# Kernel optimization log

Measured on AMD Instinct MI355X. Metric: run time of the kernel, lower is better.

Reference implementation:

```python
import jax, jax.numpy as jnp
import numpy as np

MARGIN = 1.0  # from init_kwargs
B, H, W, P = 64, 512, 640, 100000


def setup_inputs() -> dict:
    key = jax.random.key(0)
    k0, k1, k2, k3, k4, k5 = jax.random.split(key, 6)
    return {
        "inp": jax.random.normal(k0, (B, 1, H, W), dtype=jnp.float32),
        "x_A": jax.random.randint(k1, (B, P), 0, W, dtype=jnp.int32),
        "y_A": jax.random.randint(k2, (B, P), 0, H, dtype=jnp.int32),
        "x_B": jax.random.randint(k3, (B, P), 0, W, dtype=jnp.int32),
        "y_B": jax.random.randint(k4, (B, P), 0, H, dtype=jnp.int32),
        "ordinal": jax.random.randint(k5, (B, P), 0, 3, dtype=jnp.int32),
    }


def reference(inp, x_A, y_A, x_B, y_B, ordinal):
    # inp: [B,1,H,W]; point coords: [B,P]; ordinal in {0,1,2} -> gt in {-1,0,1}
    depth = inp[:, 0]                                   # [B,H,W]
    bidx = jnp.arange(depth.shape[0])[:, None]          # [B,1]
    z_A = depth[bidx, y_A, x_A]                         # [B,P] gather
    z_B = depth[bidx, y_B, x_B]                         # [B,P] gather
    gt = (ordinal - 1).astype(depth.dtype)              # {-1,0,1}
    mask = jnp.abs(gt)
    zd = z_A - z_B
    m = jnp.asarray(MARGIN, depth.dtype)
    # ordered pairs: log(1+exp(-min(gt*zd, m))); equal pairs: max(zd^2, m^2)
    loss = mask * jnp.log(1.0 + jnp.exp(-jnp.minimum(gt * zd, m))) \
         + (1.0 - mask) * jnp.maximum(zd * zd, m * m)
    n_point_total = depth.shape[0] * x_A.shape[1]
    return jnp.sum(loss) / n_point_total
```

## Files before the change

kernel.cpp:

```cpp
#include <hip/hip_runtime.h>


constexpr int B = 64;
constexpr int H = 512;
constexpr int W = 640;
constexpr int P = 100000;
constexpr int SEGS = 8;
constexpr int SEGP = P / SEGS;
constexpr int NT = 512;
constexpr int G4 = SEGP / 4;
constexpr int KG = (G4 + NT - 1) / NT;
constexpr int TAIL_T = G4 - (KG - 1) * NT;
constexpr int KS = KG * 4;
constexpr int SROWS = 48;
constexpr int NS = (H + SROWS - 1) / SROWS;
constexpr int SELEMS = SROWS * W;
constexpr int LELEMS = (H - (NS - 1) * SROWS) * W;
constexpr int PF = SELEMS / (NT * 4);
constexpr int PF_LAST = LELEMS / (NT * 4);
constexpr int NBLK = B * SEGS;
constexpr float INV_N = 1.0f / (float)(B * P);

typedef float vfloat4 __attribute__((ext_vector_type(4)));
typedef int vint4 __attribute__((ext_vector_type(4)));

__device__ __forceinline__ unsigned bf16_rnd(float f) {
    return (__builtin_bit_cast(unsigned, f) + 0x8000u) >> 16;
}

__global__ __attribute__((amdgpu_flat_work_group_size(NT, NT),
                          amdgpu_waves_per_eu(2, 2)))
void rdc_kernel(
        const float* __restrict__ depth,
        const vint4* __restrict__ xA4, const vint4* __restrict__ yA4,
        const vint4* __restrict__ xB4, const vint4* __restrict__ yB4,
        const vint4* __restrict__ ord4,
        float* __restrict__ partials) {
    __shared__ unsigned short stripe[SELEMS];
    __shared__ float wsum[8];

    int j = blockIdx.x;
    int x = j & 7;
    int g = j >> 3;
    int b = ((g >> 3) << 3) | x;
    int c = g & 7;
    int t = threadIdx.x;

    const float* slab = depth + (size_t)b * (H * W);
    int base_i4 = (b * P + c * SEGP) >> 2;

    int offA[KS], offB[KS];
    unsigned zAB[KS];
    unsigned rankW = 0u;
    unsigned signW = 0u;
    #pragma unroll
    for (int k = 0; k < KG; ++k) {
        int gl = k * NT + t;
        if (k == KG - 1 && gl >= G4) gl = G4 - 1;
        int gi = base_i4 + gl;
        vint4 xa = __builtin_nontemporal_load(&xA4[gi]);
        vint4 ya = __builtin_nontemporal_load(&yA4[gi]);
        vint4 xb = __builtin_nontemporal_load(&xB4[gi]);
        vint4 yb = __builtin_nontemporal_load(&yB4[gi]);
        vint4 od = __builtin_nontemporal_load(&ord4[gi]);
        int s0 = 4 * k;
        offA[s0+0] = ya.x * W + xa.x;  offB[s0+0] = yb.x * W + xb.x;
        offA[s0+1] = ya.y * W + xa.y;  offB[s0+1] = yb.y * W + xb.y;
        offA[s0+2] = ya.z * W + xa.z;  offB[s0+2] = yb.z * W + xb.z;
        offA[s0+3] = ya.w * W + xa.w;  offB[s0+3] = yb.w * W + xb.w;
        rankW |= (unsigned)(od.x != 1) << (s0+0);
        rankW |= (unsigned)(od.y != 1) << (s0+1);
        rankW |= (unsigned)(od.z != 1) << (s0+2);
        rankW |= (unsigned)(od.w != 1) << (s0+3);
        signW |= (unsigned)(od.x == 2) << (s0+0);
        signW |= (unsigned)(od.y == 2) << (s0+1);
        signW |= (unsigned)(od.z == 2) << (s0+2);
        signW |= (unsigned)(od.w == 2) << (s0+3);
        zAB[s0+0] = 0u; zAB[s0+1] = 0u; zAB[s0+2] = 0u; zAB[s0+3] = 0u;
    }

    vfloat4 pf[PF];
    #pragma unroll
    for (int i = 0; i < PF; ++i)
        pf[i] = *(const vfloat4*)(slab + ((i * NT + t) << 2));
    #pragma unroll
    for (int i = 0; i < PF; ++i) {
        uint2 pk;
        pk.x = bf16_rnd(pf[i].x) | (bf16_rnd(pf[i].y) << 16);
        pk.y = bf16_rnd(pf[i].z) | (bf16_rnd(pf[i].w) << 16);
        *(uint2*)&stripe[(i * NT + t) << 2] = pk;
    }
    __syncthreads();

    for (int s = 0; s < NS; ++s) {
        int npf = (s + 1 < NS) ? ((s + 1 == NS - 1) ? PF_LAST : PF) : 0;
        int gbase = (s + 1) * SELEMS;
        #pragma unroll
        for (int i = 0; i < PF; ++i)
            if (i < npf)
                pf[i] = *(const vfloat4*)(slab + gbase + ((i * NT + t) << 2));

        unsigned base = (unsigned)(s * SELEMS);
        unsigned span = (s == NS - 1) ? (unsigned)LELEMS : (unsigned)SELEMS;
        #pragma unroll
        for (int k = 0; k < KS; ++k) {
            unsigned la = (unsigned)offA[k] - base;
            unsigned va = (unsigned)stripe[la < span ? la : 0u];
            zAB[k] = (la < span) ? ((zAB[k] & 0xFFFF0000u) | va) : zAB[k];
            unsigned lb = (unsigned)offB[k] - base;
            unsigned vb = (unsigned)stripe[lb < span ? lb : 0u];
            zAB[k] = (lb < span) ? ((zAB[k] & 0x0000FFFFu) | (vb << 16)) : zAB[k];
        }
        __syncthreads();

        if (npf) {
            #pragma unroll
            for (int i = 0; i < PF; ++i)
                if (i < npf) {
                    uint2 pk;
                    pk.x = bf16_rnd(pf[i].x) | (bf16_rnd(pf[i].y) << 16);
                    pk.y = bf16_rnd(pf[i].z) | (bf16_rnd(pf[i].w) << 16);
                    *(uint2*)&stripe[(i * NT + t) << 2] = pk;
                }
            __syncthreads();
        }
    }

    float acc = 0.0f;
    #pragma unroll
    for (int k = 0; k < KG; ++k) {
        float gmask = (k < KG - 1 || t < TAIL_T) ? 1.0f : 0.0f;
        #pragma unroll
        for (int m = 0; m < 4; ++m) {
            int s = 4 * k + m;
            float za = __builtin_bit_cast(float, zAB[s] << 16);
            float zb = __builtin_bit_cast(float, zAB[s] & 0xFFFF0000u);
            float zd = za - zb;
            unsigned rb = (rankW >> s) & 1u;
            unsigned sb = (signW >> s) & 1u;
            float gzd = sb ? zd : -zd;
            float lr = __logf(1.0f + __expf(-fminf(gzd, 1.0f)));
            float le = fmaxf(zd * zd, 1.0f);
            acc += gmask * (rb ? lr : le);
        }
    }

    #pragma unroll
    for (int o = 32; o > 0; o >>= 1)
        acc += __shfl_down(acc, o, 64);
    int lane = t & 63;
    int wid  = t >> 6;
    if (lane == 0) wsum[wid] = acc;
    __syncthreads();
    if (wid == 0 && lane == 0) {
        float v = 0.0f;
        #pragma unroll
        for (int w = 0; w < 8; ++w) v += wsum[w];
        partials[j] = v;
    }
}

__global__ __launch_bounds__(256) void rdc_finalize(
        const float* __restrict__ partials, float* __restrict__ out, int n) {
    float acc = 0.0f;
    for (int k = threadIdx.x; k < n; k += 256)
        acc += partials[k];
    #pragma unroll
    for (int o = 32; o > 0; o >>= 1)
        acc += __shfl_down(acc, o, 64);
    __shared__ float wsum[4];
    int lane = threadIdx.x & 63;
    int wid  = threadIdx.x >> 6;
    if (lane == 0) wsum[wid] = acc;
    __syncthreads();
    if (wid == 0 && lane == 0)
        out[0] = (wsum[0] + wsum[1] + wsum[2] + wsum[3]) * INV_N;
}

extern "C" void kernel_launch(void* const* d_in, const int* in_sizes, int n_in,
                              void* d_out, int out_size, void* d_ws, size_t ws_size,
                              hipStream_t stream) {
    const float* depth = (const float*)d_in[0];
    const vint4* xA4 = (const vint4*)d_in[1];
    const vint4* yA4 = (const vint4*)d_in[2];
    const vint4* xB4 = (const vint4*)d_in[3];
    const vint4* yB4 = (const vint4*)d_in[4];
    const vint4* ord4 = (const vint4*)d_in[5];
    float* out = (float*)d_out;

    float* partials = (float*)d_ws;
    rdc_kernel<<<NBLK, NT, 0, stream>>>(depth, xA4, yA4, xB4, yB4, ord4, partials);
    rdc_finalize<<<1, 256, 0, stream>>>(partials, out, NBLK);
}
```

Measured before the change: 293.5 us.

## Double-buffer bf16 depth stripes and shrink stripe height with more segments

```diff
diff --git a/kernel.cpp b/kernel.cpp
--- a/kernel.cpp
+++ b/kernel.cpp
@@ -5,19 +5,19 @@
 constexpr int H = 512;
 constexpr int W = 640;
 constexpr int P = 100000;
-constexpr int SEGS = 8;
+constexpr int SEGS = 10;
 constexpr int SEGP = P / SEGS;
 constexpr int NT = 512;
 constexpr int G4 = SEGP / 4;
 constexpr int KG = (G4 + NT - 1) / NT;
 constexpr int TAIL_T = G4 - (KG - 1) * NT;
 constexpr int KS = KG * 4;
-constexpr int SROWS = 48;
+constexpr int SROWS = 24;
 constexpr int NS = (H + SROWS - 1) / SROWS;
 constexpr int SELEMS = SROWS * W;
 constexpr int LELEMS = (H - (NS - 1) * SROWS) * W;
-constexpr int PF = SELEMS / (NT * 4);
-constexpr int PF_LAST = LELEMS / (NT * 4);
+constexpr int F4_FULL = SELEMS / 4;
+constexpr int F4_LAST = LELEMS / 4;
 constexpr int NBLK = B * SEGS;
 constexpr float INV_N = 1.0f / (float)(B * P);
 
@@ -28,25 +28,24 @@
     return (__builtin_bit_cast(unsigned, f) + 0x8000u) >> 16;
 }
 
-__global__ __attribute__((amdgpu_flat_work_group_size(NT, NT),
-                          amdgpu_waves_per_eu(2, 2)))
-void rdc_kernel(
+__global__ __launch_bounds__(NT) void rdc_kernel(
         const float* __restrict__ depth,
         const vint4* __restrict__ xA4, const vint4* __restrict__ yA4,
         const vint4* __restrict__ xB4, const vint4* __restrict__ yB4,
         const vint4* __restrict__ ord4,
         float* __restrict__ partials) {
-    __shared__ unsigned short stripe[SELEMS];
+    __shared__ unsigned short stripe[2][SELEMS];
     __shared__ float wsum[8];
 
     int j = blockIdx.x;
     int x = j & 7;
     int g = j >> 3;
-    int b = ((g >> 3) << 3) | x;
-    int c = g & 7;
+    int b = (g / SEGS) * 8 + x;
+    int c = g % SEGS;
     int t = threadIdx.x;
 
     const float* slab = depth + (size_t)b * (H * W);
+    const vfloat4* slab4 = (const vfloat4*)slab;
     int base_i4 = (b * P + c * SEGP) >> 2;
 
     int offA[KS], offB[KS];
@@ -79,51 +78,60 @@
         zAB[s0+0] = 0u; zAB[s0+1] = 0u; zAB[s0+2] = 0u; zAB[s0+3] = 0u;
     }
 
-    vfloat4 pf[PF];
-    #pragma unroll
-    for (int i = 0; i < PF; ++i)
-        pf[i] = *(const vfloat4*)(slab + ((i * NT + t) << 2));
-    #pragma unroll
-    for (int i = 0; i < PF; ++i) {
-        uint2 pk;
-        pk.x = bf16_rnd(pf[i].x) | (bf16_rnd(pf[i].y) << 16);
-        pk.y = bf16_rnd(pf[i].z) | (bf16_rnd(pf[i].w) << 16);
-        *(uint2*)&stripe[(i * NT + t) << 2] = pk;
+    vfloat4 pf[8];
+    #pragma unroll
+    for (int i = 0; i < 8; ++i) {
+        int idx = i * NT + t;
+        if (idx < F4_FULL) pf[i] = slab4[idx];
+    }
+    #pragma unroll
+    for (int i = 0; i < 8; ++i) {
+        int idx = i * NT + t;
+        if (idx < F4_FULL) {
+            uint2 pk;
+            pk.x = bf16_rnd(pf[i].x) | (bf16_rnd(pf[i].y) << 16);
+            pk.y = bf16_rnd(pf[i].z) | (bf16_rnd(pf[i].w) << 16);
+            *(uint2*)&stripe[0][idx << 2] = pk;
+        }
     }
     __syncthreads();
 
     for (int s = 0; s < NS; ++s) {
-        int npf = (s + 1 < NS) ? ((s + 1 == NS - 1) ? PF_LAST : PF) : 0;
-        int gbase = (s + 1) * SELEMS;
-        #pragma unroll
-        for (int i = 0; i < PF; ++i)
-            if (i < npf)
-                pf[i] = *(const vfloat4*)(slab + gbase + ((i * NT + t) << 2));
+        int nf4 = (s + 1 < NS) ? ((s + 1 == NS - 1) ? F4_LAST : F4_FULL) : 0;
+        int gb4 = (s + 1) * F4_FULL;
+        #pragma unroll
+        for (int i = 0; i < 8; ++i) {
+            int idx = i * NT + t;
+            if (idx < nf4) pf[i] = slab4[gb4 + idx];
+        }
 
         unsigned base = (unsigned)(s * SELEMS);
         unsigned span = (s == NS - 1) ? (unsigned)LELEMS : (unsigned)SELEMS;
+        const unsigned short* rb = stripe[s & 1];
         #pragma unroll
         for (int k = 0; k < KS; ++k) {
             unsigned la = (unsigned)offA[k] - base;
-            unsigned va = (unsigned)stripe[la < span ? la : 0u];
+            unsigned va = rb[la < span ? la : (span - 1)];
             zAB[k] = (la < span) ? ((zAB[k] & 0xFFFF0000u) | va) : zAB[k];
             unsigned lb = (unsigned)offB[k] - base;
-            unsigned vb = (unsigned)stripe[lb < span ? lb : 0u];
+            unsigned vb = rb[lb < span ? lb : (span - 1)];
             zAB[k] = (lb < span) ? ((zAB[k] & 0x0000FFFFu) | (vb << 16)) : zAB[k];
         }
-        __syncthreads();
-
-        if (npf) {
+
+        if (nf4) {
+            unsigned short* wb = stripe[(s + 1) & 1];
             #pragma unroll
-            for (int i = 0; i < PF; ++i)
-                if (i < npf) {
+            for (int i = 0; i < 8; ++i) {
+                int idx = i * NT + t;
+                if (idx < nf4) {
                     uint2 pk;
                     pk.x = bf16_rnd(pf[i].x) | (bf16_rnd(pf[i].y) << 16);
                     pk.y = bf16_rnd(pf[i].z) | (bf16_rnd(pf[i].w) << 16);
-                    *(uint2*)&stripe[(i * NT + t) << 2] = pk;
+                    *(uint2*)&wb[idx << 2] = pk;
                 }
-            __syncthreads();
-        }
+            }
+        }
+        __syncthreads();
     }
 
     float acc = 0.0f;
@@ -136,12 +144,12 @@
             float za = __builtin_bit_cast(float, zAB[s] << 16);
             float zb = __builtin_bit_cast(float, zAB[s] & 0xFFFF0000u);
             float zd = za - zb;
-            unsigned rb = (rankW >> s) & 1u;
-            unsigned sb = (signW >> s) & 1u;
-            float gzd = sb ? zd : -zd;
+            unsigned rbit = (rankW >> s) & 1u;
+            unsigned sbit = (signW >> s) & 1u;
+            float gzd = sbit ? zd : -zd;
             float lr = __logf(1.0f + __expf(-fminf(gzd, 1.0f)));
             float le = fmaxf(zd * zd, 1.0f);
-            acc += gmask * (rb ? lr : le);
+            acc += gmask * (rbit ? lr : le);
         }
     }
 
```

Measured after the change: 371.0 us. +26.4%, slower.
